# Optimization experiments

Measured on AMD Instinct MI355X. Metric: run time of the kernel, lower is better.

## Reference

```python
import jax, jax.numpy as jnp
import numpy as np

DILATIONS = (1, 6, 12, 24, 36)
EPS = 1e-5


def conv2d(x, w, dil, pad):
    # x: (N,C,H,W), w: (O,I,3,3) or (O,I,1,1)
    return jax.lax.conv_general_dilated(
        x, w, window_strides=(1, 1), padding=[(pad, pad), (pad, pad)],
        rhs_dilation=(dil, dil), dimension_numbers=('NCHW', 'OIHW', 'NCHW'))


def _bilinear_sample(img, ys, xs):
    # img: (C,H,W); ys, xs: (H,W,9) float sampling coords; zero padding outside.
    C, H, W = img.shape
    y0 = jnp.floor(ys)
    x0 = jnp.floor(xs)
    wy1 = ys - y0
    wx1 = xs - x0
    wy0 = 1.0 - wy1
    wx0 = 1.0 - wx1

    def gather(yi, xi, w):
        valid = (yi >= 0) & (yi < H) & (xi >= 0) & (xi < W)
        yc = jnp.clip(yi, 0, H - 1).astype(jnp.int32)
        xc = jnp.clip(xi, 0, W - 1).astype(jnp.int32)
        v = img[:, yc, xc]  # (C,H,W,9)
        return v * (w * valid)[None]

    return (gather(y0, x0, wy0 * wx0) + gather(y0, x0 + 1, wy0 * wx1)
            + gather(y0 + 1, x0, wy1 * wx0) + gather(y0 + 1, x0 + 1, wy1 * wx1))


def deform_unfold(x, offset, dil, pad):
    # x: (N,C,H,W), offset: (N,18,H,W) interleaved (dy,dx) per 3x3 tap.
    N, C, H, W = x.shape
    ky = jnp.repeat(jnp.arange(3), 3)  # (9,)
    kx = jnp.tile(jnp.arange(3), 3)
    base_y = (jnp.arange(H)[:, None, None] + (ky * dil - pad)).astype(x.dtype)  # (H,1,9)
    base_x = (jnp.arange(W)[None, :, None] + (kx * dil - pad)).astype(x.dtype)  # (1,W,9)
    dy = jnp.transpose(offset[:, 0::2], (0, 2, 3, 1))  # (N,H,W,9)
    dx = jnp.transpose(offset[:, 1::2], (0, 2, 3, 1))
    ys = base_y[None] + dy  # (N,H,W,9)
    xs = base_x[None] + dx
    return jax.vmap(_bilinear_sample)(x, ys, xs)  # (N,C,H,W,9)


def dynamic_head(x, cat_ws, scale_w, gamma, beta):
    N, C, H, W = x.shape
    outs = [x]
    for w, dil in zip(cat_ws, DILATIONS):
        fo = conv2d(x, w, dil, dil)           # (N,27,H,W); pad == dil keeps size
        filt = jax.nn.softmax(jnp.transpose(fo[:, :9], (0, 2, 3, 1)), axis=-1)  # (N,H,W,9)
        off = fo[:, -18:]                      # (N,18,H,W)
        samp = deform_unfold(x, off, dil, dil)  # (N,C,H,W,9)
        outs.append(jnp.einsum('nchwk,nhwk->nchw', samp, filt))
    cat = jnp.concatenate(outs, axis=1)        # (N,6C,H,W)
    y = conv2d(cat, scale_w, 1, 0)             # (N,C,H,W)
    mean = jnp.mean(y, axis=(0, 2, 3))
    var = jnp.var(y, axis=(0, 2, 3))
    y = (y - mean[None, :, None, None]) * jax.lax.rsqrt(var + EPS)[None, :, None, None]
    return y * gamma[None, :, None, None] + beta[None, :, None, None]


def setup_inputs() -> dict:
    key = jax.random.key(0)
    ks = jax.random.split(key, 8)
    C = 512
    x = jax.random.normal(ks[0], (2, C, 64, 64), dtype=jnp.float32)
    cat_ws = [0.02 * jax.random.normal(ks[1 + i], (27, C, 3, 3), dtype=jnp.float32) for i in range(5)]
    scale_w = 0.02 * jax.random.normal(ks[6], (C, 6 * C, 1, 1), dtype=jnp.float32)
    gamma = jnp.ones((C,), dtype=jnp.float32)
    beta = jnp.zeros((C,), dtype=jnp.float32)
    return {'x': x, 'w1': cat_ws[0], 'w2': cat_ws[1], 'w3': cat_ws[2],
            'w4': cat_ws[3], 'w5': cat_ws[4], 'scale_w': scale_w,
            'gamma': gamma, 'beta': beta}


def reference(x, w1, w2, w3, w4, w5, scale_w, gamma, beta):
    return dynamic_head(x, (w1, w2, w3, w4, w5), scale_w, gamma, beta)
```

## Files before the change

### kernel.cpp

```cpp
#include <hip/hip_runtime.h>

typedef short short8 __attribute__((ext_vector_type(8)));
typedef float f32x4 __attribute__((ext_vector_type(4)));

#define CST 3072

__device__ __forceinline__ float bf2f(short s) {
  unsigned u = ((unsigned)(unsigned short)s) << 16;
  return __builtin_bit_cast(float, u);
}
__device__ __forceinline__ short f2bf(float f) {
  unsigned u = __builtin_bit_cast(unsigned, f);
  u = (u + 0x7FFFu + ((u >> 16) & 1u)) >> 16;
  return (short)u;
}
__device__ __forceinline__ void gl16(const short* g, short* l) {
  __builtin_amdgcn_global_load_lds(
      (const __attribute__((address_space(1))) unsigned*)g,
      (__attribute__((address_space(3))) unsigned*)l, 16, 0, 0);
}

__global__ __launch_bounds__(256) void k_init(const float* __restrict__ x,
                                              const float* __restrict__ sw,
                                              const float* __restrict__ w1, const float* __restrict__ w2,
                                              const float* __restrict__ w3, const float* __restrict__ w4,
                                              const float* __restrict__ w5,
                                              short* __restrict__ cat,
                                              short* __restrict__ wbf, short* __restrict__ wdr,
                                              float* __restrict__ stats) {
  __shared__ float tile[64][65];
  int b = blockIdx.x;
  int t = threadIdx.x;
  if (b < 1024) {
    int cblk = b & 7, h = (b >> 3) & 63, n = b >> 9;
    int c0 = cblk * 64;
    int lw = t & 63, grp = t >> 6;
    const float* xp = x + (((size_t)n * 512 + c0) * 64 + h) * 64;
#pragma unroll
    for (int i = 0; i < 16; ++i) {
      int cl = grp * 16 + i;
      tile[cl][lw] = xp[(size_t)cl * 4096 + lw];
    }
    __syncthreads();
    int c8 = t & 7, wq = t >> 3;
    size_t mbase = ((size_t)n * 64 + h) * 64;
#pragma unroll
    for (int it = 0; it < 2; ++it) {
      int w = wq + it * 32;
      short8 o;
#pragma unroll
      for (int j = 0; j < 8; ++j) o[j] = f2bf(tile[c8 * 8 + j][w]);
      *(short8*)(cat + (mbase + w) * CST + c0 + c8 * 8) = o;
    }
  } else if (b < 1792) {
    int i8 = (b - 1024) * 256 + t;
    const float4* sp = (const float4*)(sw + (size_t)i8 * 8);
    float4 f0 = sp[0], f1 = sp[1];
    short8 o;
    o[0] = f2bf(f0.x); o[1] = f2bf(f0.y); o[2] = f2bf(f0.z); o[3] = f2bf(f0.w);
    o[4] = f2bf(f1.x); o[5] = f2bf(f1.y); o[6] = f2bf(f1.z); o[7] = f2bf(f1.w);
    *(short8*)(wbf + (size_t)i8 * 8) = o;
  } else if (b < 4672) {
    int j = (b - 1792) * 256 + t;
    int c = j & 511;
    int t2 = j >> 9;
    int oc = t2 & 31;
    int t3 = t2 >> 5;
    int tap = t3 % 9;
    int di = t3 / 9;
    float v = 0.f;
    if (oc < 27) {
      const float* wp = (di == 0) ? w1 : (di == 1) ? w2 : (di == 2) ? w3 : (di == 3) ? w4 : w5;
      v = wp[((oc * 512 + c) * 3 + tap / 3) * 3 + tap % 3];
    }
    wdr[j] = f2bf(v);
  } else {
    int idx = (b - 4672) * 256 + t;
    stats[idx] = 0.f;
  }
}

__global__ __launch_bounds__(128) void k_conv(const short* __restrict__ xsrc,
                                              const short* __restrict__ wdr_all,
                                              int* __restrict__ ctab) {
  __shared__ short As[64 * 256];
  __shared__ short Bs[32 * 256];
  float (*fo)[32][33] = (float (*)[32][33])(void*)As;
  int tid = threadIdx.x;
  int wave = tid >> 6, lane = tid & 63;
  int l15 = lane & 15, quad = lane >> 4;
  int b = blockIdx.x;
  int di = b >> 7;
  int loc = b & 127;
  const int DIL[5] = {1, 6, 12, 24, 36};
  int d = DIL[di];
  int rid = (loc & 7) * 16 + (loc >> 3);
  int h = rid & 63, n = rid >> 6;
  f32x4 acc[2][2];
  f32x4 zz = {0.f, 0.f, 0.f, 0.f};
#pragma unroll
  for (int i = 0; i < 2; ++i)
#pragma unroll
    for (int j = 0; j < 2; ++j) acc[i][j] = zz;
  const short8 z8 = {0, 0, 0, 0, 0, 0, 0, 0};
  int aoff[16];
  int boff[8];
#pragma unroll
  for (int i = 0; i < 16; ++i) {
    int q = i * 128 + tid;
    int w = q >> 5, ch = q & 31;
    aoff[i] = w * CST + (ch ^ (w & 7)) * 8;
  }
#pragma unroll
  for (int i = 0; i < 8; ++i) {
    int q = i * 128 + tid;
    int oc = q >> 5, ch = q & 31;
    boff[i] = oc * 512 + (ch ^ (oc & 7)) * 8;
  }
  const short* wbase = wdr_all + (size_t)di * 9 * 32 * 512;
  int rowb = (n << 12);
#pragma unroll 1
  for (int kh = 0; kh < 2; ++kh) {
    int lastty = -1;
#pragma unroll
    for (int tap = 0; tap < 9; ++tap) {
      int ty = tap / 3, tx = tap % 3;
      int hh = h + (ty - 1) * d;
      if ((unsigned)hh >= 64u) continue;
      __syncthreads();
      if (ty != lastty) {
        const short* abase = xsrc + (size_t)(rowb + (hh << 6)) * CST + kh * 256;
#pragma unroll
        for (int i = 0; i < 16; ++i)
          gl16(abase + aoff[i], As + (i * 128 + wave * 64) * 8);
        lastty = ty;
      }
      {
        const short* bbase = wbase + tap * 32 * 512 + kh * 256;
#pragma unroll
        for (int i = 0; i < 8; ++i)
          gl16(bbase + boff[i], Bs + (i * 128 + wave * 64) * 8);
      }
      __syncthreads();
      int s0 = wave * 32 + (tx - 1) * d;
#pragma unroll
      for (int ks = 0; ks < 8; ++ks) {
        int c = ks * 4 + quad;
        short8 a[2], bb[2];
#pragma unroll
        for (int mt = 0; mt < 2; ++mt) {
          int wp = s0 + mt * 16 + l15;
          bool ok = (unsigned)wp < 64u;
          int wc = ok ? wp : 0;
          short8 av = *(const short8*)(As + wc * 256 + (c ^ (wc & 7)) * 8);
          a[mt] = ok ? av : z8;
        }
#pragma unroll
        for (int ot = 0; ot < 2; ++ot) {
          int oc = ot * 16 + l15;
          bb[ot] = *(const short8*)(Bs + oc * 256 + (c ^ (oc & 7)) * 8);
        }
#pragma unroll
        for (int mt = 0; mt < 2; ++mt)
#pragma unroll
          for (int ot = 0; ot < 2; ++ot)
            acc[mt][ot] = __builtin_amdgcn_mfma_f32_16x16x32_bf16(a[mt], bb[ot], acc[mt][ot], 0, 0, 0);
      }
    }
  }
  __syncthreads();
#pragma unroll
  for (int mt = 0; mt < 2; ++mt)
#pragma unroll
    for (int ot = 0; ot < 2; ++ot)
#pragma unroll
      for (int r = 0; r < 4; ++r)
        fo[wave][mt * 16 + quad * 4 + r][ot * 16 + l15] = acc[mt][ot][r];
  __syncthreads();
  if (tid < 64) {
    int p = tid;
    float* fp = fo[p >> 5][p & 31];
    float mx = fp[0];
#pragma unroll
    for (int k = 1; k < 9; ++k) mx = fmaxf(mx, fp[k]);
    float s = 0.f, e[9];
#pragma unroll
    for (int k = 0; k < 9; ++k) { e[k] = __expf(fp[k] - mx); s += e[k]; }
    float inv = 1.f / s;
#pragma unroll
    for (int k = 0; k < 9; ++k) fp[k] = e[k] * inv;
  }
  __syncthreads();
#pragma unroll
  for (int rr = 0; rr < 5; ++rr) {
    int task = rr * 128 + tid;
    if (task < 576) {
      int p = task / 9;
      int k = task - p * 9;
      const float* fp = fo[p >> 5][p & 31];
      float f = fp[k];
      float dy = fp[9 + 2 * k];
      float dx = fp[10 + 2 * k];
      float ys = (float)(h + (k / 3 - 1) * d) + dy;
      float xs = (float)(p + (k % 3 - 1) * d) + dx;
      float y0f = floorf(ys), x0f = floorf(xs);
      float wy1 = ys - y0f, wx1 = xs - x0f;
      float wy0 = 1.f - wy1, wx0 = 1.f - wx1;
      int y0 = (int)y0f, x0 = (int)x0f;
      int4 ent;
      int* ep = (int*)&ent;
#pragma unroll
      for (int cy = 0; cy < 2; ++cy)
#pragma unroll
        for (int cx = 0; cx < 2; ++cx) {
          int yy = y0 + cy, xx = x0 + cx;
          bool v = ((unsigned)yy < 64u) && ((unsigned)xx < 64u);
          float wt = f * (cy ? wy1 : wy0) * (cx ? wx1 : wx0);
          int row = v ? (yy * 64 + xx) : 0;
          unsigned wb = v ? (unsigned)(unsigned short)f2bf(wt) : 0u;
          ep[cy * 2 + cx] = row | (int)(wb << 16);
        }
      int mm = rowb + (h << 6) + p;
      ((int4*)ctab)[((size_t)di * 8192 + mm) * 9 + k] = ent;
    }
  }
}

__global__ __launch_bounds__(256, 4) void k_samp(const short* __restrict__ xsrc,
                                                 short* __restrict__ cat,
                                                 const int* __restrict__ ctab) {
  int tid = threadIdx.x;
  int wv = __builtin_amdgcn_readfirstlane(tid >> 6);
  int lane = tid & 63;
  int b = blockIdx.x;
  int di = b >> 11;
  int loc = b & 2047;
  int m = (loc & 7) * 1024 + (loc >> 3) * 4 + wv;
  int n = m >> 12;
  const int4* tp = (const int4*)ctab + ((size_t)di * 8192 + m) * 9;
  const short* xb = xsrc + (size_t)(n << 12) * CST + lane * 8;
  float acc[8] = {0.f, 0.f, 0.f, 0.f, 0.f, 0.f, 0.f, 0.f};
#pragma unroll
  for (int k = 0; k < 9; ++k) {
    int4 e = tp[k];
    const int* ep = (const int*)&e;
#pragma unroll
    for (int c = 0; c < 4; ++c) {
      int dw = ep[c];
      float wt = __builtin_bit_cast(float, (unsigned)dw & 0xFFFF0000u);
      int row = dw & 0xFFFF;
      const short8 vv = *(const short8*)(xb + (size_t)row * CST);
#pragma unroll
      for (int j = 0; j < 8; ++j) acc[j] += wt * bf2f(vv[j]);
    }
  }
  short8 o8;
#pragma unroll
  for (int j = 0; j < 8; ++j) o8[j] = f2bf(acc[j]);
  *(short8*)(cat + (size_t)m * CST + 512 * (di + 1) + lane * 8) = o8;
}

__global__ __launch_bounds__(512, 2) void k_gemm(const short* __restrict__ A,
                                                 const short* __restrict__ B,
                                                 short* __restrict__ Y) {
  __shared__ short As[2][128 * 64];
  __shared__ short Bs[2][256 * 64];
  int tid = threadIdx.x;
  int wave = tid >> 6, lane = tid & 63;
  int l15 = lane & 15, quad = lane >> 4;
  int bid = blockIdx.x;
  int xcd = bid & 7, g = bid >> 3;
  int mt = xcd * 8 + (g & 7);
  int nt = (g >> 3) & 1;
  int s  = g >> 4;
  int m0 = mt * 128, n0 = nt * 256;
  int kbeg = s * 1536;
  int wm = (wave >> 2) * 64;
  int wn = (wave & 3) * 64;
  f32x4 acc[4][4];
  f32x4 zz = {0.f, 0.f, 0.f, 0.f};
#pragma unroll
  for (int i = 0; i < 4; ++i)
#pragma unroll
    for (int j = 0; j < 4; ++j) acc[i][j] = zz;
  int r6 = tid >> 3, c8 = tid & 7;
  int cs = (c8 ^ (r6 & 7)) * 8;
  const short* asrc = A + (size_t)(m0 + r6) * CST + kbeg + cs;
  const short* bsrc = B + (size_t)(n0 + r6) * CST + kbeg + cs;
  short* adst = &As[0][0] + tid * 8;
  short* bdst = &Bs[0][0] + tid * 8;
#define STAGE_A(p, u, kc) gl16(asrc + (size_t)(u) * 64 * CST + (kc), adst + (p) * 8192 + (u) * 4096)
#define STAGE_B(p, u, kc) gl16(bsrc + (size_t)(u) * 64 * CST + (kc), bdst + (p) * 16384 + (u) * 4096)
  STAGE_A(0, 0, 0); STAGE_A(0, 1, 0);
  STAGE_B(0, 0, 0); STAGE_B(0, 1, 0); STAGE_B(0, 2, 0); STAGE_B(0, 3, 0);
  STAGE_A(1, 0, 64); STAGE_A(1, 1, 64);
  STAGE_B(1, 0, 64); STAGE_B(1, 1, 64); STAGE_B(1, 2, 64); STAGE_B(1, 3, 64);
#pragma unroll 1
  for (int t = 0; t < 24; ++t) {
    int cur = t & 1;
    if (t == 23) { asm volatile("s_waitcnt vmcnt(0)" ::: "memory"); }
    else         { asm volatile("s_waitcnt vmcnt(6)" ::: "memory"); }
    __builtin_amdgcn_s_barrier();
    __builtin_amdgcn_sched_barrier(0);
    const short* Ab = &As[cur][0];
    const short* Bb = &Bs[cur][0];
    short8 a[4][2], bl[2][2];
#pragma unroll
    for (int i = 0; i < 4; ++i) {
      int row = wm + i * 16 + l15;
      const short* rp = Ab + row * 64;
#pragma unroll
      for (int kk = 0; kk < 2; ++kk)
        a[i][kk] = *(const short8*)(rp + ((quad + kk * 4) ^ (row & 7)) * 8);
    }
#pragma unroll
    for (int j = 0; j < 2; ++j) {
      int row = wn + j * 16 + l15;
      const short* rp = Bb + row * 64;
#pragma unroll
      for (int kk = 0; kk < 2; ++kk)
        bl[j][kk] = *(const short8*)(rp + ((quad + kk * 4) ^ (row & 7)) * 8);
    }
    __builtin_amdgcn_s_barrier();
    asm volatile("s_waitcnt lgkmcnt(0)" ::: "memory");
    __builtin_amdgcn_sched_barrier(0);
    __builtin_amdgcn_s_setprio(1);
#pragma unroll
    for (int kk = 0; kk < 2; ++kk)
#pragma unroll
      for (int i = 0; i < 4; ++i)
#pragma unroll
        for (int j = 0; j < 2; ++j)
          acc[i][j] = __builtin_amdgcn_mfma_f32_16x16x32_bf16(a[i][kk], bl[j][kk], acc[i][j], 0, 0, 0);
    __builtin_amdgcn_s_setprio(0);
    __builtin_amdgcn_s_barrier();
    __builtin_amdgcn_sched_barrier(0);
    short8 bh[2][2];
#pragma unroll
    for (int j = 0; j < 2; ++j) {
      int row = wn + 32 + j * 16 + l15;
      const short* rp = Bb + row * 64;
#pragma unroll
      for (int kk = 0; kk < 2; ++kk)
        bh[j][kk] = *(const short8*)(rp + ((quad + kk * 4) ^ (row & 7)) * 8);
    }
    if (t < 22) {
      int kc = (t + 2) * 64;
      STAGE_A(cur, 0, kc); STAGE_A(cur, 1, kc);
    }
    __builtin_amdgcn_s_barrier();
    asm volatile("s_waitcnt lgkmcnt(0)" ::: "memory");
    __builtin_amdgcn_sched_barrier(0);
    __builtin_amdgcn_s_setprio(1);
#pragma unroll
    for (int kk = 0; kk < 2; ++kk)
#pragma unroll
      for (int i = 0; i < 4; ++i)
#pragma unroll
        for (int j = 0; j < 2; ++j)
          acc[i][j + 2] = __builtin_amdgcn_mfma_f32_16x16x32_bf16(a[i][kk], bh[j][kk], acc[i][j + 2], 0, 0, 0);
    __builtin_amdgcn_s_setprio(0);
    __builtin_amdgcn_s_barrier();
    __builtin_amdgcn_sched_barrier(0);
    if (t < 22) {
      int kc = (t + 2) * 64;
      STAGE_B(cur, 0, kc); STAGE_B(cur, 1, kc); STAGE_B(cur, 2, kc); STAGE_B(cur, 3, kc);
    }
  }
#undef STAGE_A
#undef STAGE_B
  short* Yp = Y + (size_t)s * (8192 * 512);
#pragma unroll
  for (int i = 0; i < 4; ++i) {
    int row = m0 + wm + i * 16 + quad * 4;
#pragma unroll
    for (int j = 0; j < 4; ++j) {
      int col = n0 + wn + j * 16 + l15;
#pragma unroll
      for (int r = 0; r < 4; ++r)
        Yp[(size_t)(row + r) * 512 + col] = f2bf(acc[i][j][r]);
    }
  }
}

__global__ __launch_bounds__(256) void k_stats(const short* __restrict__ Y,
                                               float* __restrict__ stats) {
  __shared__ float ls[1024];
  const short* Y1 = Y + (size_t)8192 * 512;
  int tid = threadIdx.x;
  int c8 = (tid & 63) * 8;
  int rg = tid >> 6;
  int row0 = blockIdx.x * 32 + rg * 8;
  float s[8], q[8];
#pragma unroll
  for (int j = 0; j < 8; ++j) { s[j] = 0.f; q[j] = 0.f; }
  for (int r = 0; r < 8; ++r) {
    size_t ro = (size_t)(row0 + r) * 512 + c8;
    short8 a = *(const short8*)(Y + ro);
    short8 bb = *(const short8*)(Y1 + ro);
#pragma unroll
    for (int j = 0; j < 8; ++j) {
      float v = bf2f(a[j]) + bf2f(bb[j]);
      s[j] += v; q[j] += v * v;
    }
  }
  for (int i = tid; i < 1024; i += 256) ls[i] = 0.f;
  __syncthreads();
#pragma unroll
  for (int j = 0; j < 8; ++j) {
    atomicAdd(&ls[c8 + j], s[j]);
    atomicAdd(&ls[512 + c8 + j], q[j]);
  }
  __syncthreads();
  for (int i = tid; i < 1024; i += 256) atomicAdd(&stats[i], ls[i]);
}

__global__ __launch_bounds__(256) void k_norm(const short* __restrict__ Y,
                                              const float* __restrict__ stats,
                                              const float* __restrict__ gamma,
                                              const float* __restrict__ beta,
                                              float* __restrict__ out) {
  __shared__ float tile[64][65];
  const short* Y1 = Y + (size_t)8192 * 512;
  int b = blockIdx.x;
  int cblk = b & 7, h = (b >> 3) & 63, n = b >> 9;
  int c0 = cblk * 64;
  int t = threadIdx.x;
  size_t mbase = ((size_t)n * 64 + h) * 64;
  int c8 = t & 7, wq = t >> 3;
#pragma unroll
  for (int it = 0; it < 2; ++it) {
    int w = wq + it * 32;
    size_t ro = (mbase + w) * 512 + c0 + c8 * 8;
    short8 a = *(const short8*)(Y + ro);
    short8 bb = *(const short8*)(Y1 + ro);
#pragma unroll
    for (int j = 0; j < 8; ++j) tile[w][c8 * 8 + j] = bf2f(a[j]) + bf2f(bb[j]);
  }
  __syncthreads();
  int w4 = (t & 15) * 4, cg = t >> 4;
  float* op = out + (((size_t)n * 512 + c0) * 64 + h) * 64;
#pragma unroll
  for (int i = 0; i < 4; ++i) {
    int c2 = cg * 4 + i;
    int cc = c0 + c2;
    float mean = stats[cc] * (1.f / 8192.f);
    float var = stats[512 + cc] * (1.f / 8192.f) - mean * mean;
    float Ai = gamma[cc] * rsqrtf(var + 1e-5f);
    float Bi = beta[cc] - mean * Ai;
    float4 o;
    o.x = tile[w4 + 0][c2] * Ai + Bi;
    o.y = tile[w4 + 1][c2] * Ai + Bi;
    o.z = tile[w4 + 2][c2] * Ai + Bi;
    o.w = tile[w4 + 3][c2] * Ai + Bi;
    *(float4*)(op + (size_t)c2 * 4096 + w4) = o;
  }
}

extern "C" void kernel_launch(void* const* d_in, const int* in_sizes, int n_in,
                              void* d_out, int out_size, void* d_ws, size_t ws_size,
                              hipStream_t stream) {
  const float* x  = (const float*)d_in[0];
  const float* w1 = (const float*)d_in[1];
  const float* w2 = (const float*)d_in[2];
  const float* w3 = (const float*)d_in[3];
  const float* w4 = (const float*)d_in[4];
  const float* w5 = (const float*)d_in[5];
  const float* sw = (const float*)d_in[6];
  const float* gamma = (const float*)d_in[7];
  const float* beta  = (const float*)d_in[8];
  float* out = (float*)d_out;

  char* ws = (char*)d_ws;
  short* cat   = (short*)ws;
  short* wbf   = (short*)(ws + 50331648);
  short* wdr   = (short*)(ws + 53477376);
  short* yb    = (short*)(ws + 54951936);
  float* stats = (float*)(ws + 71729152);
  int*   ctab  = (int*)(ws + 71733248);

  k_init<<<4676, 256, 0, stream>>>(x, sw, w1, w2, w3, w4, w5, cat, wbf, wdr, stats);
  k_conv<<<640, 128, 0, stream>>>(cat, wdr, ctab);
  k_samp<<<10240, 256, 0, stream>>>(cat, cat, ctab);
  k_gemm<<<256, 512, 0, stream>>>(cat, wbf, yb);
  k_stats<<<256, 256, 0, stream>>>(yb, stats);
  k_norm<<<1024, 256, 0, stream>>>(yb, stats, gamma, beta, out);
}
```

Measured before the change: 219.4 us.

## Drop split-K in final GEMM and fuse batch-norm statistics into its epilogue

The 1x1 scale GEMM now uses 128x128 output tiles over the full K=3072 instead of 128x256 tiles with a two-way split-K. Each tile writes one bf16 Y buffer and accumulates per-channel sum and sum-of-squares from the fp32 accumulators, via LDS atomics and then global atomics. This removes the k_stats kernel and the second partial buffer read in k_norm. In exchange each block runs twice as many K iterations, and B-tile reuse per block is lower. The statistics now come from fp32 values rather than the rounded bf16 output.

```diff
diff --git a/kernel.cpp b/kernel.cpp
--- a/kernel.cpp
+++ b/kernel.cpp
@@ -262,49 +262,47 @@
 
 __global__ __launch_bounds__(512, 2) void k_gemm(const short* __restrict__ A,
                                                  const short* __restrict__ B,
-                                                 short* __restrict__ Y) {
+                                                 short* __restrict__ Y,
+                                                 float* __restrict__ stats) {
   __shared__ short As[2][128 * 64];
-  __shared__ short Bs[2][256 * 64];
+  __shared__ short Bs[2][128 * 64];
+  __shared__ float sred[128][2];
   int tid = threadIdx.x;
   int wave = tid >> 6, lane = tid & 63;
   int l15 = lane & 15, quad = lane >> 4;
   int bid = blockIdx.x;
   int xcd = bid & 7, g = bid >> 3;
   int mt = xcd * 8 + (g & 7);
-  int nt = (g >> 3) & 1;
-  int s  = g >> 4;
-  int m0 = mt * 128, n0 = nt * 256;
-  int kbeg = s * 1536;
+  int nt = g >> 3;
+  int m0 = mt * 128, n0 = nt * 128;
   int wm = (wave >> 2) * 64;
-  int wn = (wave & 3) * 64;
-  f32x4 acc[4][4];
+  int wn = (wave & 3) * 32;
+  f32x4 acc[4][2];
   f32x4 zz = {0.f, 0.f, 0.f, 0.f};
 #pragma unroll
   for (int i = 0; i < 4; ++i)
 #pragma unroll
-    for (int j = 0; j < 4; ++j) acc[i][j] = zz;
+    for (int j = 0; j < 2; ++j) acc[i][j] = zz;
   int r6 = tid >> 3, c8 = tid & 7;
   int cs = (c8 ^ (r6 & 7)) * 8;
-  const short* asrc = A + (size_t)(m0 + r6) * CST + kbeg + cs;
-  const short* bsrc = B + (size_t)(n0 + r6) * CST + kbeg + cs;
+  const short* asrc = A + (size_t)(m0 + r6) * CST + cs;
+  const short* bsrc = B + (size_t)(n0 + r6) * CST + cs;
   short* adst = &As[0][0] + tid * 8;
   short* bdst = &Bs[0][0] + tid * 8;
 #define STAGE_A(p, u, kc) gl16(asrc + (size_t)(u) * 64 * CST + (kc), adst + (p) * 8192 + (u) * 4096)
-#define STAGE_B(p, u, kc) gl16(bsrc + (size_t)(u) * 64 * CST + (kc), bdst + (p) * 16384 + (u) * 4096)
-  STAGE_A(0, 0, 0); STAGE_A(0, 1, 0);
-  STAGE_B(0, 0, 0); STAGE_B(0, 1, 0); STAGE_B(0, 2, 0); STAGE_B(0, 3, 0);
-  STAGE_A(1, 0, 64); STAGE_A(1, 1, 64);
-  STAGE_B(1, 0, 64); STAGE_B(1, 1, 64); STAGE_B(1, 2, 64); STAGE_B(1, 3, 64);
+#define STAGE_B(p, u, kc) gl16(bsrc + (size_t)(u) * 64 * CST + (kc), bdst + (p) * 8192 + (u) * 4096)
+  STAGE_A(0, 0, 0); STAGE_A(0, 1, 0); STAGE_B(0, 0, 0); STAGE_B(0, 1, 0);
+  STAGE_A(1, 0, 64); STAGE_A(1, 1, 64); STAGE_B(1, 0, 64); STAGE_B(1, 1, 64);
 #pragma unroll 1
-  for (int t = 0; t < 24; ++t) {
+  for (int t = 0; t < 48; ++t) {
     int cur = t & 1;
-    if (t == 23) { asm volatile("s_waitcnt vmcnt(0)" ::: "memory"); }
-    else         { asm volatile("s_waitcnt vmcnt(6)" ::: "memory"); }
+    if (t == 47) { asm volatile("s_waitcnt vmcnt(0)" ::: "memory"); }
+    else         { asm volatile("s_waitcnt vmcnt(4)" ::: "memory"); }
     __builtin_amdgcn_s_barrier();
     __builtin_amdgcn_sched_barrier(0);
     const short* Ab = &As[cur][0];
     const short* Bb = &Bs[cur][0];
-    short8 a[4][2], bl[2][2];
+    short8 a[4][2], bf[2][2];
 #pragma unroll
     for (int i = 0; i < 4; ++i) {
       int row = wm + i * 16 + l15;
@@ -319,38 +317,17 @@
       const short* rp = Bb + row * 64;
 #pragma unroll
       for (int kk = 0; kk < 2; ++kk)
-        bl[j][kk] = *(const short8*)(rp + ((quad + kk * 4) ^ (row & 7)) * 8);
-    }
-    __builtin_amdgcn_s_barrier();
+        bf[j][kk] = *(const short8*)(rp + ((quad + kk * 4) ^ (row & 7)) * 8);
+    }
     asm volatile("s_waitcnt lgkmcnt(0)" ::: "memory");
     __builtin_amdgcn_sched_barrier(0);
-    __builtin_amdgcn_s_setprio(1);
-#pragma unroll
-    for (int kk = 0; kk < 2; ++kk)
-#pragma unroll
-      for (int i = 0; i < 4; ++i)
-#pragma unroll
-        for (int j = 0; j < 2; ++j)
-          acc[i][j] = __builtin_amdgcn_mfma_f32_16x16x32_bf16(a[i][kk], bl[j][kk], acc[i][j], 0, 0, 0);
-    __builtin_amdgcn_s_setprio(0);
     __builtin_amdgcn_s_barrier();
     __builtin_amdgcn_sched_barrier(0);
-    short8 bh[2][2];
-#pragma unroll
-    for (int j = 0; j < 2; ++j) {
-      int row = wn + 32 + j * 16 + l15;
-      const short* rp = Bb + row * 64;
-#pragma unroll
-      for (int kk = 0; kk < 2; ++kk)
-        bh[j][kk] = *(const short8*)(rp + ((quad + kk * 4) ^ (row & 7)) * 8);
-    }
-    if (t < 22) {
+    if (t < 46) {
       int kc = (t + 2) * 64;
       STAGE_A(cur, 0, kc); STAGE_A(cur, 1, kc);
-    }
-    __builtin_amdgcn_s_barrier();
-    asm volatile("s_waitcnt lgkmcnt(0)" ::: "memory");
-    __builtin_amdgcn_sched_barrier(0);
+      STAGE_B(cur, 0, kc); STAGE_B(cur, 1, kc);
+    }
     __builtin_amdgcn_s_setprio(1);
 #pragma unroll
     for (int kk = 0; kk < 2; ++kk)
@@ -358,61 +335,43 @@
       for (int i = 0; i < 4; ++i)
 #pragma unroll
         for (int j = 0; j < 2; ++j)
-          acc[i][j + 2] = __builtin_amdgcn_mfma_f32_16x16x32_bf16(a[i][kk], bh[j][kk], acc[i][j + 2], 0, 0, 0);
+          acc[i][j] = __builtin_amdgcn_mfma_f32_16x16x32_bf16(a[i][kk], bf[j][kk], acc[i][j], 0, 0, 0);
     __builtin_amdgcn_s_setprio(0);
-    __builtin_amdgcn_s_barrier();
-    __builtin_amdgcn_sched_barrier(0);
-    if (t < 22) {
-      int kc = (t + 2) * 64;
-      STAGE_B(cur, 0, kc); STAGE_B(cur, 1, kc); STAGE_B(cur, 2, kc); STAGE_B(cur, 3, kc);
-    }
   }
 #undef STAGE_A
 #undef STAGE_B
-  short* Yp = Y + (size_t)s * (8192 * 512);
+  if (tid < 256) ((float*)sred)[tid] = 0.f;
+  __syncthreads();
 #pragma unroll
   for (int i = 0; i < 4; ++i) {
     int row = m0 + wm + i * 16 + quad * 4;
 #pragma unroll
-    for (int j = 0; j < 4; ++j) {
+    for (int j = 0; j < 2; ++j) {
       int col = n0 + wn + j * 16 + l15;
 #pragma unroll
       for (int r = 0; r < 4; ++r)
-        Yp[(size_t)(row + r) * 512 + col] = f2bf(acc[i][j][r]);
-    }
-  }
-}
-
-__global__ __launch_bounds__(256) void k_stats(const short* __restrict__ Y,
-                                               float* __restrict__ stats) {
-  __shared__ float ls[1024];
-  const short* Y1 = Y + (size_t)8192 * 512;
-  int tid = threadIdx.x;
-  int c8 = (tid & 63) * 8;
-  int rg = tid >> 6;
-  int row0 = blockIdx.x * 32 + rg * 8;
-  float s[8], q[8];
-#pragma unroll
-  for (int j = 0; j < 8; ++j) { s[j] = 0.f; q[j] = 0.f; }
-  for (int r = 0; r < 8; ++r) {
-    size_t ro = (size_t)(row0 + r) * 512 + c8;
-    short8 a = *(const short8*)(Y + ro);
-    short8 bb = *(const short8*)(Y1 + ro);
-#pragma unroll
-    for (int j = 0; j < 8; ++j) {
-      float v = bf2f(a[j]) + bf2f(bb[j]);
-      s[j] += v; q[j] += v * v;
-    }
-  }
-  for (int i = tid; i < 1024; i += 256) ls[i] = 0.f;
-  __syncthreads();
-#pragma unroll
-  for (int j = 0; j < 8; ++j) {
-    atomicAdd(&ls[c8 + j], s[j]);
-    atomicAdd(&ls[512 + c8 + j], q[j]);
-  }
-  __syncthreads();
-  for (int i = tid; i < 1024; i += 256) atomicAdd(&stats[i], ls[i]);
+        Y[(size_t)(row + r) * 512 + col] = f2bf(acc[i][j][r]);
+    }
+  }
+#pragma unroll
+  for (int j = 0; j < 2; ++j) {
+    float s = 0.f, q = 0.f;
+#pragma unroll
+    for (int i = 0; i < 4; ++i)
+#pragma unroll
+      for (int r = 0; r < 4; ++r) {
+        float v = acc[i][j][r];
+        s += v; q += v * v;
+      }
+    int lc = wn + j * 16 + l15;
+    atomicAdd(&sred[lc][0], s);
+    atomicAdd(&sred[lc][1], q);
+  }
+  __syncthreads();
+  if (tid < 128) {
+    atomicAdd(&stats[n0 + tid], sred[tid][0]);
+    atomicAdd(&stats[512 + n0 + tid], sred[tid][1]);
+  }
 }
 
 __global__ __launch_bounds__(256) void k_norm(const short* __restrict__ Y,
@@ -421,7 +380,6 @@
                                               const float* __restrict__ beta,
                                               float* __restrict__ out) {
   __shared__ float tile[64][65];
-  const short* Y1 = Y + (size_t)8192 * 512;
   int b = blockIdx.x;
   int cblk = b & 7, h = (b >> 3) & 63, n = b >> 9;
   int c0 = cblk * 64;
@@ -433,9 +391,8 @@
     int w = wq + it * 32;
     size_t ro = (mbase + w) * 512 + c0 + c8 * 8;
     short8 a = *(const short8*)(Y + ro);
-    short8 bb = *(const short8*)(Y1 + ro);
-#pragma unroll
-    for (int j = 0; j < 8; ++j) tile[w][c8 * 8 + j] = bf2f(a[j]) + bf2f(bb[j]);
+#pragma unroll
+    for (int j = 0; j < 8; ++j) tile[w][c8 * 8 + j] = bf2f(a[j]);
   }
   __syncthreads();
   int w4 = (t & 15) * 4, cg = t >> 4;
@@ -482,7 +439,6 @@
   k_init<<<4676, 256, 0, stream>>>(x, sw, w1, w2, w3, w4, w5, cat, wbf, wdr, stats);
   k_conv<<<640, 128, 0, stream>>>(cat, wdr, ctab);
   k_samp<<<10240, 256, 0, stream>>>(cat, cat, ctab);
-  k_gemm<<<256, 512, 0, stream>>>(cat, wbf, yb);
-  k_stats<<<256, 256, 0, stream>>>(yb, stats);
+  k_gemm<<<256, 512, 0, stream>>>(cat, wbf, yb, stats);
   k_norm<<<1024, 256, 0, stream>>>(yb, stats, gamma, beta, out);
 }
```

After: 206.3 us, median of 2. 6.0% less time.
